# Kernel tuning notes

Hardware: AMD Instinct MI355X
Metric: run time of the kernel (lower is better)

Reference implementation:

```python
import math
import jax, jax.numpy as jnp
import numpy as np

L, H, C, T_MAX, V = 4, 12, 768, 1024, 50257
D = C // H
EPS = 1e-5


def setup_inputs() -> dict:
    key = jax.random.key(0)
    ks = iter(jax.random.split(key, 32))
    s = 0.02
    inp = {
        "idx": jax.random.randint(next(ks), (2, 1024), 0, V, dtype=jnp.int32),
        "wte": jax.random.normal(next(ks), (V, C), jnp.float32) * s,
        "wpe": jax.random.normal(next(ks), (T_MAX, C), jnp.float32) * s,
        # per-layer stacked params, weights stored [in, out]
        "ln1_w": jnp.ones((L, C), jnp.float32),
        "ln1_b": jnp.zeros((L, C), jnp.float32),
        "qkv_w": jax.random.normal(next(ks), (L, C, 3 * C), jnp.float32) * s,
        "qkv_b": jnp.zeros((L, 3 * C), jnp.float32),
        "proj_w": jax.random.normal(next(ks), (L, C, C), jnp.float32) * (s / math.sqrt(2 * L)),
        "proj_b": jnp.zeros((L, C), jnp.float32),
        "ln2_w": jnp.ones((L, C), jnp.float32),
        "ln2_b": jnp.zeros((L, C), jnp.float32),
        "fc_w": jax.random.normal(next(ks), (L, C, 4 * C), jnp.float32) * s,
        "fc_b": jnp.zeros((L, 4 * C), jnp.float32),
        "fc2_w": jax.random.normal(next(ks), (L, 4 * C, C), jnp.float32) * (s / math.sqrt(2 * L)),
        "fc2_b": jnp.zeros((L, C), jnp.float32),
        "lnf_w": jnp.ones((C,), jnp.float32),
        "lnf_b": jnp.zeros((C,), jnp.float32),
        "head_w": jax.random.normal(next(ks), (C, V), jnp.float32) * s,
    }
    return inp


def _layernorm(x, w, b):
    mu = jnp.mean(x, axis=-1, keepdims=True)
    var = jnp.mean(jnp.square(x - mu), axis=-1, keepdims=True)
    return (x - mu) * jax.lax.rsqrt(var + EPS) * w + b


def _new_gelu(x):
    k = math.sqrt(2.0 / math.pi)
    return 0.5 * x * (1.0 + jnp.tanh(k * (x + 0.044715 * x * x * x)))


def _gpt_forward(idx, wte, wpe, layer_params, lnf_w, lnf_b, head_w):
    B, T = idx.shape
    x = wte[idx] + wpe[:T][None, :, :]  # [B, T, C]
    causal = jnp.tril(jnp.ones((T, T), bool))

    def block(x, p):
        ln1w, ln1b, qkvw, qkvb, pw, pb, ln2w, ln2b, fcw, fcb, fc2w, fc2b = p
        h = _layernorm(x, ln1w, ln1b)
        qkv = h @ qkvw + qkvb  # [B, T, 3C]
        q, k, v = jnp.split(qkv, 3, axis=-1)
        # [B, H, T, D]
        q = q.reshape(B, T, H, D).transpose(0, 2, 1, 3)
        k = k.reshape(B, T, H, D).transpose(0, 2, 1, 3)
        v = v.reshape(B, T, H, D).transpose(0, 2, 1, 3)
        att = jnp.einsum("bhtd,bhsd->bhts", q, k) * (1.0 / math.sqrt(D))
        att = jnp.where(causal, att, -jnp.inf)
        att = jax.nn.softmax(att, axis=-1)
        y = jnp.einsum("bhts,bhsd->bhtd", att, v)
        y = y.transpose(0, 2, 1, 3).reshape(B, T, C)
        x = x + (y @ pw + pb)
        h2 = _layernorm(x, ln2w, ln2b)
        m = _new_gelu(h2 @ fcw + fcb) @ fc2w + fc2b
        return x + m, None

    x, _ = jax.lax.scan(block, x, layer_params)
    x = _layernorm(x, lnf_w, lnf_b)
    logits = x @ head_w  # [B, T, V]
    return logits.reshape(B * T, V)


def reference(idx, wte, wpe, ln1_w, ln1_b, qkv_w, qkv_b, proj_w, proj_b,
              ln2_w, ln2_b, fc_w, fc_b, fc2_w, fc2_b, lnf_w, lnf_b, head_w):
    layer_params = (ln1_w, ln1_b, qkv_w, qkv_b, proj_w, proj_b,
                    ln2_w, ln2_b, fc_w, fc_b, fc2_w, fc2_b)
    return _gpt_forward(idx, wte, wpe, layer_params, lnf_w, lnf_b, head_w)
```

## Files before the change

kernel.cpp:

```cpp
#include <hip/hip_runtime.h>
#include <hip/hip_bf16.h>

typedef __hip_bfloat16 bf16;
typedef __attribute__((ext_vector_type(8))) short bf16x8;
typedef __attribute__((ext_vector_type(4))) float f32x4;
typedef __attribute__((ext_vector_type(4), aligned(4))) float f32x4u;

#define NL 4
#define NH 12
#define C 768
#define T 1024
#define NB 2
#define BTOK 2048
#define V 50257
#define DH 64

__device__ __forceinline__ void gload16(const void* g, void* l) {
  __builtin_amdgcn_global_load_lds(
      (const __attribute__((address_space(1))) void*)g,
      (__attribute__((address_space(3))) void*)l, 16, 0, 0);
}

__device__ __forceinline__ float block_sum(float v, float* red) {
#pragma unroll
  for (int off = 32; off; off >>= 1) v += __shfl_down(v, off);
  int lane = threadIdx.x & 63, wid = threadIdx.x >> 6;
  __syncthreads();
  if (lane == 0) red[wid] = v;
  __syncthreads();
  return red[0] + red[1] + red[2] + red[3];
}

__global__ __launch_bounds__(256) void k_embed(const int* __restrict__ idx,
    const float* __restrict__ wte, const float* __restrict__ wpe,
    float* __restrict__ x) {
  long i = (long)blockIdx.x * 256 + threadIdx.x;
  int bt = (int)(i / C), c = (int)(i % C);
  int t = bt & (T - 1);
  x[i] = wte[(long)idx[bt] * C + c] + wpe[(long)t * C + c];
}

__global__ __launch_bounds__(256) void k_transpose_bf16(const float* __restrict__ W,
    bf16* __restrict__ Wt, int K, int N) {
  __shared__ float tile[32][33];
  long zoff = (long)blockIdx.z * K * N;
  W += zoff;
  Wt += zoff;
  int n0 = blockIdx.x * 32, k0 = blockIdx.y * 32;
  int tx = threadIdx.x, ty = threadIdx.y;
#pragma unroll
  for (int i = 0; i < 4; i++) {
    int k = k0 + ty + i * 8, n = n0 + tx;
    if (k < K && n < N) tile[ty + i * 8][tx] = W[(long)k * N + n];
  }
  __syncthreads();
#pragma unroll
  for (int i = 0; i < 4; i++) {
    int n = n0 + ty + i * 8, k = k0 + tx;
    if (n < N && k < K) Wt[(long)n * K + k] = __float2bfloat16(tile[tx][ty + i * 8]);
  }
}

__global__ __launch_bounds__(256) void k_layernorm(const float* __restrict__ x,
    const float* __restrict__ w, const float* __restrict__ b, bf16* __restrict__ out) {
  __shared__ float red[4];
  long row = blockIdx.x;
  const float* xr = x + row * C;
  int t = threadIdx.x;
  float v0 = xr[t], v1 = xr[t + 256], v2 = xr[t + 512];
  float s = block_sum(v0 + v1 + v2, red);
  float mu = s * (1.0f / C);
  float d0 = v0 - mu, d1 = v1 - mu, d2 = v2 - mu;
  float vs = block_sum(d0 * d0 + d1 * d1 + d2 * d2, red);
  float inv = rsqrtf(vs * (1.0f / C) + 1e-5f);
  bf16* orow = out + row * C;
  orow[t]       = __float2bfloat16(d0 * inv * w[t]       + b[t]);
  orow[t + 256] = __float2bfloat16(d1 * inv * w[t + 256] + b[t + 256]);
  orow[t + 512] = __float2bfloat16(d2 * inv * w[t + 512] + b[t + 512]);
}

__global__ __launch_bounds__(256) void k_attn(const bf16* __restrict__ q,
    const bf16* __restrict__ k, const bf16* __restrict__ vt,
    bf16* __restrict__ yb) {
  __shared__ __align__(16) bf16 Pl[4][16][72];
  int pr = blockIdx.x, bh = blockIdx.y;
  int b = bh / NH, h = bh % NH;
  int tid = threadIdx.x, w = tid >> 6, lane = tid & 63;
  int l15 = lane & 15, hi = lane >> 4;
  const bf16* qbase = q + (long)bh * T * DH;
  const bf16* kbase = k + (long)bh * T * DH;
  const bf16* vbase = vt + (long)bh * DH * T;

  for (int s2 = 0; s2 < 2; s2++) {
    int qt = s2 ? (T / 64 - 1 - pr) : pr;
    int qrow = qt * 64 + w * 16 + l15;
    bf16x8 qf0 = *(const bf16x8*)(qbase + (long)qrow * DH + hi * 8);
    bf16x8 qf1 = *(const bf16x8*)(qbase + (long)qrow * DH + 32 + hi * 8);

    f32x4 accy[4] = {};
    float m_run = -1e30f, l_run = 0.f;

    int nkt = qt + 1;
    for (int kt = 0; kt < nkt; kt++) {
      int kv0 = kt * 64;
      f32x4 accs[4] = {};
#pragma unroll
      for (int kvi = 0; kvi < 4; kvi++) {
        const bf16* kr = kbase + (long)(kv0 + kvi * 16 + l15) * DH + hi * 8;
        bf16x8 kf0 = *(const bf16x8*)kr;
        bf16x8 kf1 = *(const bf16x8*)(kr + 32);
        accs[kvi] = __builtin_amdgcn_mfma_f32_16x16x32_bf16(kf0, qf0, accs[kvi], 0, 0, 0);
        accs[kvi] = __builtin_amdgcn_mfma_f32_16x16x32_bf16(kf1, qf1, accs[kvi], 0, 0, 0);
      }
      bool diag = (kt == qt);
      float p[4][4];
      float tmax = -1e30f;
#pragma unroll
      for (int kvi = 0; kvi < 4; kvi++)
#pragma unroll
        for (int rr = 0; rr < 4; rr++) {
          float s = accs[kvi][rr];
          if (diag && (kvi * 16 + hi * 4 + rr > w * 16 + l15)) s = -1e30f;
          p[kvi][rr] = s;
          tmax = fmaxf(tmax, s);
        }
      tmax = fmaxf(tmax, __shfl_xor(tmax, 16));
      tmax = fmaxf(tmax, __shfl_xor(tmax, 32));
      float m_new = fmaxf(m_run, tmax);
      float scl = __expf(m_run - m_new);
      float psum = 0.f;
#pragma unroll
      for (int kvi = 0; kvi < 4; kvi++)
#pragma unroll
        for (int rr = 0; rr < 4; rr++) {
          float e = __expf(p[kvi][rr] - m_new);
          p[kvi][rr] = e;
          psum += e;
        }
      psum += __shfl_xor(psum, 16);
      psum += __shfl_xor(psum, 32);
      l_run = l_run * scl + psum;
      m_run = m_new;
#pragma unroll
      for (int rr = 0; rr < 4; rr++) {
        float sy = __shfl(scl, hi * 4 + rr);
#pragma unroll
        for (int j = 0; j < 4; j++) accy[j][rr] *= sy;
      }
#pragma unroll
      for (int kvi = 0; kvi < 4; kvi++) {
        union { bf16 hh[2]; unsigned u; } pk0, pk1;
        pk0.hh[0] = __float2bfloat16(p[kvi][0]);
        pk0.hh[1] = __float2bfloat16(p[kvi][1]);
        pk1.hh[0] = __float2bfloat16(p[kvi][2]);
        pk1.hh[1] = __float2bfloat16(p[kvi][3]);
        *(unsigned*)&Pl[w][l15][kvi * 16 + hi * 4]     = pk0.u;
        *(unsigned*)&Pl[w][l15][kvi * 16 + hi * 4 + 2] = pk1.u;
      }
#pragma unroll
      for (int c = 0; c < 2; c++) {
        bf16x8 pf = *(const bf16x8*)&Pl[w][l15][c * 32 + hi * 8];
#pragma unroll
        for (int j = 0; j < 4; j++) {
          const bf16* vr = vbase + (long)(j * 16 + l15) * T + kv0 + c * 32 + hi * 8;
          bf16x8 vf = *(const bf16x8*)vr;
          accy[j] = __builtin_amdgcn_mfma_f32_16x16x32_bf16(pf, vf, accy[j], 0, 0, 0);
        }
      }
    }
    float inv = 1.0f / l_run;
#pragma unroll
    for (int rr = 0; rr < 4; rr++) {
      float li = __shfl(inv, hi * 4 + rr);
      int qg = qt * 64 + w * 16 + hi * 4 + rr;
#pragma unroll
      for (int j = 0; j < 4; j++)
        yb[((long)(b * T + qg)) * C + h * DH + j * 16 + l15] =
            __float2bfloat16(accy[j][rr] * li);
    }
  }
}

__global__ __launch_bounds__(512, 1) void k_head(const bf16* __restrict__ A,
    const bf16* __restrict__ B, float* __restrict__ Cv) {
  __shared__ __align__(16) char lds[131072];
  int hw = blockIdx.y * 8 + blockIdx.x;
  int L = (hw & 7) * 197 + (hw >> 3);
  int mt = L & 7, nt = L >> 3;
  int m0 = mt * 256, n0 = nt * 256;
  int tid = threadIdx.x, lane = tid & 63, wid = tid >> 6;
  int wm = wid >> 2, wn = wid & 3;
  int l15 = lane & 15, hi = lane >> 4, l7 = lane & 7;
  int sg = (lane & 7) ^ (lane >> 3);
  int srA = wid * 8 + (lane >> 3);
  const bf16* Ab = A + (long)(m0 + srA) * 768 + sg * 8;
  const bf16* Bb = B + (long)(n0 + srA) * 768 + sg * 8;
  auto STAGE = [&](int tile, int h) {
    char* dst = lds + (tile & 1) * 65536 + h * 16384 + wid * 1024;
    const bf16* src = (h < 2 ? Ab : Bb) + (long)((h & 1) * 128) * 768 + tile * 64;
    gload16(src, dst);
    gload16(src + 64 * 768, dst + 8192);
  };
  f32x4 acc[8][4] = {};
  STAGE(0, 0); STAGE(0, 1); STAGE(0, 2); STAGE(0, 3); STAGE(1, 0);
  asm volatile("s_waitcnt vmcnt(2)" ::: "memory");
  __builtin_amdgcn_s_barrier();
  int bro = (wn & 1) * 64;
  int g0 = (hi ^ l7) * 16, g1 = ((4 + hi) ^ l7) * 16;
  for (int t = 0; t < 12; t++) {
    char* ha = lds + (t & 1) * 65536 + wm * 16384;
    char* hb = lds + (t & 1) * 65536 + 32768 + (wn >> 1) * 16384;
    bf16x8 af[4], bv[4];
#pragma unroll
    for (int mf = 0; mf < 4; mf++)
      af[mf] = *(const bf16x8*)(ha + (mf * 16 + l15) * 128 + g0);
#pragma unroll
    for (int nf = 0; nf < 4; nf++)
      bv[nf] = *(const bf16x8*)(hb + (bro + nf * 16 + l15) * 128 + g0);
    if (t + 1 < 12) { STAGE(t + 1, 1); STAGE(t + 1, 2); }
    __builtin_amdgcn_s_barrier();
    __builtin_amdgcn_s_setprio(1);
#pragma unroll
    for (int mf = 0; mf < 4; mf++)
#pragma unroll
      for (int nf = 0; nf < 4; nf++)
        acc[mf][nf] = __builtin_amdgcn_mfma_f32_16x16x32_bf16(af[mf], bv[nf], acc[mf][nf], 0, 0, 0);
    __builtin_amdgcn_s_setprio(0);
    __builtin_amdgcn_s_barrier();
#pragma unroll
    for (int mf = 0; mf < 4; mf++)
      af[mf] = *(const bf16x8*)(ha + ((mf + 4) * 16 + l15) * 128 + g0);
    if (t + 1 < 12) STAGE(t + 1, 3);
    __builtin_amdgcn_s_barrier();
    __builtin_amdgcn_s_setprio(1);
#pragma unroll
    for (int mf = 0; mf < 4; mf++)
#pragma unroll
      for (int nf = 0; nf < 4; nf++)
        acc[mf + 4][nf] = __builtin_amdgcn_mfma_f32_16x16x32_bf16(af[mf], bv[nf], acc[mf + 4][nf], 0, 0, 0);
    __builtin_amdgcn_s_setprio(0);
    __builtin_amdgcn_s_barrier();
#pragma unroll
    for (int mf = 0; mf < 4; mf++)
      af[mf] = *(const bf16x8*)(ha + (mf * 16 + l15) * 128 + g1);
#pragma unroll
    for (int nf = 0; nf < 4; nf++)
      bv[nf] = *(const bf16x8*)(hb + (bro + nf * 16 + l15) * 128 + g1);
    __builtin_amdgcn_s_barrier();
    __builtin_amdgcn_s_setprio(1);
#pragma unroll
    for (int mf = 0; mf < 4; mf++)
#pragma unroll
      for (int nf = 0; nf < 4; nf++)
        acc[mf][nf] = __builtin_amdgcn_mfma_f32_16x16x32_bf16(af[mf], bv[nf], acc[mf][nf], 0, 0, 0);
    __builtin_amdgcn_s_setprio(0);
    __builtin_amdgcn_s_barrier();
#pragma unroll
    for (int mf = 0; mf < 4; mf++)
      af[mf] = *(const bf16x8*)(ha + ((mf + 4) * 16 + l15) * 128 + g1);
    if (t + 2 < 12) STAGE(t + 2, 0);
    __builtin_amdgcn_s_barrier();
    __builtin_amdgcn_s_setprio(1);
#pragma unroll
    for (int mf = 0; mf < 4; mf++)
#pragma unroll
      for (int nf = 0; nf < 4; nf++)
        acc[mf + 4][nf] = __builtin_amdgcn_mfma_f32_16x16x32_bf16(af[mf], bv[nf], acc[mf + 4][nf], 0, 0, 0);
    __builtin_amdgcn_s_setprio(0);
    if (t < 11) {
      if (t + 2 < 12) asm volatile("s_waitcnt vmcnt(2)" ::: "memory");
      else            asm volatile("s_waitcnt vmcnt(0)" ::: "memory");
      __builtin_amdgcn_s_barrier();
    }
  }
  __syncthreads();
  float* Cst = (float*)lds;
#pragma unroll
  for (int rnd = 0; rnd < 4; rnd++) {
#pragma unroll
    for (int mfl = 0; mfl < 2; mfl++) {
      int mf = rnd * 2 + mfl;
#pragma unroll
      for (int nf = 0; nf < 4; nf++)
#pragma unroll
        for (int rr = 0; rr < 4; rr++)
          Cst[(wm * 32 + mfl * 16 + hi * 4 + rr) * 260 + wn * 64 + nf * 16 + l15] =
              acc[mf][nf][rr];
    }
    __syncthreads();
#pragma unroll
    for (int s = 0; s < 8; s++) {
      int gid = tid + s * 512;
      int r = gid >> 6, g = gid & 63;
      int grow = m0 + (r >> 5) * 128 + (rnd * 2 + ((r >> 4) & 1)) * 16 + (r & 15);
      int gcol = n0 + g * 4;
      f32x4 vv = *(const f32x4*)&Cst[r * 260 + g * 4];
      float* dst = Cv + (long)grow * V + gcol;
      if (gcol + 3 < V) {
        *(f32x4u*)dst = vv;
      } else {
#pragma unroll
        for (int e = 0; e < 4; e++)
          if (gcol + e < V) dst[e] = vv[e];
      }
    }
    __syncthreads();
  }
}

#define SBK 64
template <int EPI>
__global__ __launch_bounds__(256) void k_gemm_s(const bf16* __restrict__ A,
    const bf16* __restrict__ B, const float* __restrict__ bias,
    void* __restrict__ Cv, int M, int N, int K, int lda, int ldb, int ldc,
    void* __restrict__ Cv2, void* __restrict__ Cv3) {
  __shared__ __align__(16) bf16 As[2][64][SBK];
  __shared__ __align__(16) bf16 Bs[2][128][SBK];
  int nwg = gridDim.x * gridDim.y;
  int hw = blockIdx.y * gridDim.x + blockIdx.x;
  int logical = (hw & 7) * (nwg >> 3) + (hw >> 3);
  int bx = logical % gridDim.x, by = logical / gridDim.x;
  int m0 = bx * 64, n0 = by * 128;
  int tid = threadIdx.x;
  int lane = tid & 63, w = tid >> 6;
  int l15 = lane & 15, hi = lane >> 4, l7 = lane & 7;
  int srow = lane >> 3;
  int sgr = lane & 7;
  int scol = ((sgr ^ srow) << 3);
  f32x4 acc[4][2] = {};
  const bf16* Ag = A + (long)(m0 + w * 8 + srow) * lda + scol;
  const bf16* Bg = B + (long)(n0 + w * 8 + srow) * ldb + scol;
  int NT = K / SBK;
  auto STAGE = [&](int t) {
    int k0 = t * SBK, b = t & 1;
    gload16(Ag + k0,            &As[b][w * 8][0]);
    gload16(Ag + k0 + 32 * lda, &As[b][w * 8 + 32][0]);
    gload16(Bg + k0,            &Bs[b][w * 8][0]);
    gload16(Bg + k0 + 32 * ldb, &Bs[b][w * 8 + 32][0]);
    gload16(Bg + k0 + 64 * ldb, &Bs[b][w * 8 + 64][0]);
    gload16(Bg + k0 + 96 * ldb, &Bs[b][w * 8 + 96][0]);
  };
  STAGE(0);
  STAGE(1);
  int c0 = (hi ^ l7) << 3, c1 = ((4 + hi) ^ l7) << 3;
  for (int t = 0; t < NT; t++) {
    int b = t & 1;
    if (t + 1 < NT) asm volatile("s_waitcnt vmcnt(6)" ::: "memory");
    else            asm volatile("s_waitcnt vmcnt(0)" ::: "memory");
    __builtin_amdgcn_s_barrier();
    bf16x8 a0[4], a1[4], b0[2], b1[2];
#pragma unroll
    for (int i = 0; i < 4; i++) {
      a0[i] = *(const bf16x8*)&As[b][i * 16 + l15][c0];
      a1[i] = *(const bf16x8*)&As[b][i * 16 + l15][c1];
    }
#pragma unroll
    for (int j = 0; j < 2; j++) {
      b0[j] = *(const bf16x8*)&Bs[b][w * 32 + j * 16 + l15][c0];
      b1[j] = *(const bf16x8*)&Bs[b][w * 32 + j * 16 + l15][c1];
    }
    asm volatile("s_waitcnt lgkmcnt(0)" ::: "memory");
    __builtin_amdgcn_s_barrier();
    if (t + 2 < NT) STAGE(t + 2);
    __builtin_amdgcn_s_setprio(1);
#pragma unroll
    for (int i = 0; i < 4; i++)
#pragma unroll
      for (int j = 0; j < 2; j++) {
        acc[i][j] = __builtin_amdgcn_mfma_f32_16x16x32_bf16(a0[i], b0[j], acc[i][j], 0, 0, 0);
        acc[i][j] = __builtin_amdgcn_mfma_f32_16x16x32_bf16(a1[i], b1[j], acc[i][j], 0, 0, 0);
      }
    __builtin_amdgcn_s_setprio(0);
  }
#pragma unroll
  for (int j = 0; j < 2; j++) {
    int gn = n0 + w * 32 + j * 16 + l15;
    float bv = bias[gn];
#pragma unroll
    for (int i = 0; i < 4; i++)
#pragma unroll
      for (int rr = 0; rr < 4; rr++) {
        int gm = m0 + i * 16 + hi * 4 + rr;
        float v = acc[i][j][rr] + bv;
        if constexpr (EPI == 3) {
          long off = (long)gm * ldc + gn;
          ((float*)Cv)[off] = v + ((float*)Cv)[off];
        } else if constexpr (EPI == 2) {
          float u = 0.7978845608028654f * (v + 0.044715f * v * v * v);
          u = fminf(fmaxf(u, -15.f), 15.f);
          float e2 = __expf(2.f * u);
          float th = (e2 - 1.f) / (e2 + 1.f);
          ((bf16*)Cv)[(long)gm * ldc + gn] = __float2bfloat16(0.5f * v * (1.f + th));
        } else if constexpr (EPI == 5) {
          int gb = gm >> 10, gt = gm & 1023;
          int which = gn / C;
          int r = gn - which * C;
          int h = r >> 6, d = r & 63;
          long bh = (long)(gb * NH + h);
          if (which == 0)
            ((bf16*)Cv)[(bh * T + gt) * DH + d] = __float2bfloat16(v * 0.125f);
          else if (which == 1)
            ((bf16*)Cv2)[(bh * T + gt) * DH + d] = __float2bfloat16(v);
          else
            ((bf16*)Cv3)[(bh * DH + d) * T + gt] = __float2bfloat16(v);
        }
      }
  }
}

extern "C" void kernel_launch(void* const* d_in, const int* in_sizes, int n_in,
                              void* d_out, int out_size, void* d_ws, size_t ws_size,
                              hipStream_t stream) {
  const int*   idx    = (const int*)d_in[0];
  const float* wte    = (const float*)d_in[1];
  const float* wpe    = (const float*)d_in[2];
  const float* ln1_w  = (const float*)d_in[3];
  const float* ln1_b  = (const float*)d_in[4];
  const float* qkv_w  = (const float*)d_in[5];
  const float* qkv_b  = (const float*)d_in[6];
  const float* proj_w = (const float*)d_in[7];
  const float* proj_b = (const float*)d_in[8];
  const float* ln2_w  = (const float*)d_in[9];
  const float* ln2_b  = (const float*)d_in[10];
  const float* fc_w   = (const float*)d_in[11];
  const float* fc_b   = (const float*)d_in[12];
  const float* fc2_w  = (const float*)d_in[13];
  const float* fc2_b  = (const float*)d_in[14];
  const float* lnf_w  = (const float*)d_in[15];
  const float* lnf_b  = (const float*)d_in[16];
  const float* head_w = (const float*)d_in[17];
  (void)in_sizes; (void)n_in; (void)out_size; (void)ws_size;

  char* base = (char*)d_ws;
  size_t off = 0;
  auto alloc = [&](size_t bytes) -> void* {
    void* p = base + off;
    off = (off + bytes + 255) & ~(size_t)255;
    return p;
  };
  bf16* wt_qkv  = (bf16*)alloc((size_t)NL * 3 * C * C * 2);
  bf16* wt_proj = (bf16*)alloc((size_t)NL * C * C * 2);
  bf16* wt_fc   = (bf16*)alloc((size_t)NL * 4 * C * C * 2);
  bf16* wt_fc2  = (bf16*)alloc((size_t)NL * 4 * C * C * 2);
  bf16* wt_head = (bf16*)alloc((size_t)V * C * 2);
  float* x      = (float*)alloc((size_t)BTOK * C * 4);
  bf16*  xb     = (bf16*)alloc((size_t)BTOK * C * 2);
  bf16*  qb     = (bf16*)alloc((size_t)NB * NH * T * DH * 2);
  bf16*  kb     = (bf16*)alloc((size_t)NB * NH * T * DH * 2);
  bf16*  vtb    = (bf16*)alloc((size_t)NB * NH * T * DH * 2);
  bf16*  yb     = (bf16*)alloc((size_t)BTOK * C * 2);
  bf16*  mbuf   = (bf16*)alloc((size_t)BTOK * 4 * C * 2);

  dim3 tb(32, 8);
  k_transpose_bf16<<<dim3(72, 24, NL), tb, 0, stream>>>(qkv_w, wt_qkv, C, 3 * C);
  k_transpose_bf16<<<dim3(24, 24, NL), tb, 0, stream>>>(proj_w, wt_proj, C, C);
  k_transpose_bf16<<<dim3(96, 24, NL), tb, 0, stream>>>(fc_w, wt_fc, C, 4 * C);
  k_transpose_bf16<<<dim3(24, 96, NL), tb, 0, stream>>>(fc2_w, wt_fc2, 4 * C, C);
  k_transpose_bf16<<<dim3((V + 31) / 32, 24, 1), tb, 0, stream>>>(head_w, wt_head, C, V);

  k_embed<<<BTOK * C / 256, 256, 0, stream>>>(idx, wte, wpe, x);

  for (int l = 0; l < NL; l++) {
    k_layernorm<<<BTOK, 256, 0, stream>>>(x, ln1_w + l * C, ln1_b + l * C, xb);
    k_gemm_s<5><<<dim3(32, 18), 256, 0, stream>>>(xb, wt_qkv + (long)l * 3 * C * C,
        qkv_b + l * 3 * C, qb, BTOK, 3 * C, C, C, C, 0, kb, vtb);
    k_attn<<<dim3(T / 128, NB * NH), 256, 0, stream>>>(qb, kb, vtb, yb);
    k_gemm_s<3><<<dim3(32, 6), 256, 0, stream>>>(yb, wt_proj + (long)l * C * C,
        proj_b + l * C, x, BTOK, C, C, C, C, C, nullptr, nullptr);
    k_layernorm<<<BTOK, 256, 0, stream>>>(x, ln2_w + l * C, ln2_b + l * C, xb);
    k_gemm_s<2><<<dim3(32, 24), 256, 0, stream>>>(xb, wt_fc + (long)l * 4 * C * C,
        fc_b + l * 4 * C, mbuf, BTOK, 4 * C, C, C, C, 4 * C, nullptr, nullptr);
    k_gemm_s<3><<<dim3(32, 6), 256, 0, stream>>>(mbuf, wt_fc2 + (long)l * 4 * C * C,
        fc2_b + l * C, x, BTOK, C, 4 * C, 4 * C, 4 * C, C, nullptr, nullptr);
  }
  k_layernorm<<<BTOK, 256, 0, stream>>>(x, lnf_w, lnf_b, xb);
  k_head<<<dim3(8, 197), 512, 0, stream>>>(xb, wt_head, (float*)d_out);
}
```

Measured before the change: 1.073 ms.

## Split attention causal pairs across grid z and replace head GEMM with 128x128 tiles

The attention kernel stops looping over two query tiles per block and puts each one in its own block via a third grid dimension, which doubles the block count and raises parallelism. The large 256x256 LM-head GEMM kernel (512 threads, one block per CU, 128KB LDS) is replaced by a simpler 128x128 tile kernel using 256 threads with launch bounds allowing two blocks per CU. That kernel uses a double-buffered global-to-LDS pipeline and an LDS-staged epilogue. The smaller head tiles give more blocks and occupancy but less reuse per block, and the separate attention blocks lose the load balancing that pairing short and long causal tiles provided.

```diff
diff --git a/kernel.cpp b/kernel.cpp
--- a/kernel.cpp
+++ b/kernel.cpp
@@ -91,217 +91,176 @@
   const bf16* kbase = k + (long)bh * T * DH;
   const bf16* vbase = vt + (long)bh * DH * T;
 
-  for (int s2 = 0; s2 < 2; s2++) {
-    int qt = s2 ? (T / 64 - 1 - pr) : pr;
-    int qrow = qt * 64 + w * 16 + l15;
-    bf16x8 qf0 = *(const bf16x8*)(qbase + (long)qrow * DH + hi * 8);
-    bf16x8 qf1 = *(const bf16x8*)(qbase + (long)qrow * DH + 32 + hi * 8);
-
-    f32x4 accy[4] = {};
-    float m_run = -1e30f, l_run = 0.f;
-
-    int nkt = qt + 1;
-    for (int kt = 0; kt < nkt; kt++) {
-      int kv0 = kt * 64;
-      f32x4 accs[4] = {};
-#pragma unroll
-      for (int kvi = 0; kvi < 4; kvi++) {
-        const bf16* kr = kbase + (long)(kv0 + kvi * 16 + l15) * DH + hi * 8;
-        bf16x8 kf0 = *(const bf16x8*)kr;
-        bf16x8 kf1 = *(const bf16x8*)(kr + 32);
-        accs[kvi] = __builtin_amdgcn_mfma_f32_16x16x32_bf16(kf0, qf0, accs[kvi], 0, 0, 0);
-        accs[kvi] = __builtin_amdgcn_mfma_f32_16x16x32_bf16(kf1, qf1, accs[kvi], 0, 0, 0);
-      }
-      bool diag = (kt == qt);
-      float p[4][4];
-      float tmax = -1e30f;
-#pragma unroll
-      for (int kvi = 0; kvi < 4; kvi++)
-#pragma unroll
-        for (int rr = 0; rr < 4; rr++) {
-          float s = accs[kvi][rr];
-          if (diag && (kvi * 16 + hi * 4 + rr > w * 16 + l15)) s = -1e30f;
-          p[kvi][rr] = s;
-          tmax = fmaxf(tmax, s);
-        }
-      tmax = fmaxf(tmax, __shfl_xor(tmax, 16));
-      tmax = fmaxf(tmax, __shfl_xor(tmax, 32));
-      float m_new = fmaxf(m_run, tmax);
-      float scl = __expf(m_run - m_new);
-      float psum = 0.f;
-#pragma unroll
-      for (int kvi = 0; kvi < 4; kvi++)
-#pragma unroll
-        for (int rr = 0; rr < 4; rr++) {
-          float e = __expf(p[kvi][rr] - m_new);
-          p[kvi][rr] = e;
-          psum += e;
-        }
-      psum += __shfl_xor(psum, 16);
-      psum += __shfl_xor(psum, 32);
-      l_run = l_run * scl + psum;
-      m_run = m_new;
+  int qt = blockIdx.z ? (T / 64 - 1 - pr) : pr;
+  int qrow = qt * 64 + w * 16 + l15;
+  bf16x8 qf0 = *(const bf16x8*)(qbase + (long)qrow * DH + hi * 8);
+  bf16x8 qf1 = *(const bf16x8*)(qbase + (long)qrow * DH + 32 + hi * 8);
+
+  f32x4 accy[4] = {};
+  float m_run = -1e30f, l_run = 0.f;
+
+  int nkt = qt + 1;
+  for (int kt = 0; kt < nkt; kt++) {
+    int kv0 = kt * 64;
+    f32x4 accs[4] = {};
+#pragma unroll
+    for (int kvi = 0; kvi < 4; kvi++) {
+      const bf16* kr = kbase + (long)(kv0 + kvi * 16 + l15) * DH + hi * 8;
+      bf16x8 kf0 = *(const bf16x8*)kr;
+      bf16x8 kf1 = *(const bf16x8*)(kr + 32);
+      accs[kvi] = __builtin_amdgcn_mfma_f32_16x16x32_bf16(kf0, qf0, accs[kvi], 0, 0, 0);
+      accs[kvi] = __builtin_amdgcn_mfma_f32_16x16x32_bf16(kf1, qf1, accs[kvi], 0, 0, 0);
+    }
+    bool diag = (kt == qt);
+    float p[4][4];
+    float tmax = -1e30f;
+#pragma unroll
+    for (int kvi = 0; kvi < 4; kvi++)
 #pragma unroll
       for (int rr = 0; rr < 4; rr++) {
-        float sy = __shfl(scl, hi * 4 + rr);
-#pragma unroll
-        for (int j = 0; j < 4; j++) accy[j][rr] *= sy;
-      }
-#pragma unroll
-      for (int kvi = 0; kvi < 4; kvi++) {
-        union { bf16 hh[2]; unsigned u; } pk0, pk1;
-        pk0.hh[0] = __float2bfloat16(p[kvi][0]);
-        pk0.hh[1] = __float2bfloat16(p[kvi][1]);
-        pk1.hh[0] = __float2bfloat16(p[kvi][2]);
-        pk1.hh[1] = __float2bfloat16(p[kvi][3]);
-        *(unsigned*)&Pl[w][l15][kvi * 16 + hi * 4]     = pk0.u;
-        *(unsigned*)&Pl[w][l15][kvi * 16 + hi * 4 + 2] = pk1.u;
-      }
-#pragma unroll
-      for (int c = 0; c < 2; c++) {
-        bf16x8 pf = *(const bf16x8*)&Pl[w][l15][c * 32 + hi * 8];
-#pragma unroll
-        for (int j = 0; j < 4; j++) {
-          const bf16* vr = vbase + (long)(j * 16 + l15) * T + kv0 + c * 32 + hi * 8;
-          bf16x8 vf = *(const bf16x8*)vr;
-          accy[j] = __builtin_amdgcn_mfma_f32_16x16x32_bf16(pf, vf, accy[j], 0, 0, 0);
-        }
-      }
-    }
-    float inv = 1.0f / l_run;
+        float s = accs[kvi][rr];
+        if (diag && (kvi * 16 + hi * 4 + rr > w * 16 + l15)) s = -1e30f;
+        p[kvi][rr] = s;
+        tmax = fmaxf(tmax, s);
+      }
+    tmax = fmaxf(tmax, __shfl_xor(tmax, 16));
+    tmax = fmaxf(tmax, __shfl_xor(tmax, 32));
+    float m_new = fmaxf(m_run, tmax);
+    float scl = __expf(m_run - m_new);
+    float psum = 0.f;
+#pragma unroll
+    for (int kvi = 0; kvi < 4; kvi++)
+#pragma unroll
+      for (int rr = 0; rr < 4; rr++) {
+        float e = __expf(p[kvi][rr] - m_new);
+        p[kvi][rr] = e;
+        psum += e;
+      }
+    psum += __shfl_xor(psum, 16);
+    psum += __shfl_xor(psum, 32);
+    l_run = l_run * scl + psum;
+    m_run = m_new;
 #pragma unroll
     for (int rr = 0; rr < 4; rr++) {
-      float li = __shfl(inv, hi * 4 + rr);
-      int qg = qt * 64 + w * 16 + hi * 4 + rr;
-#pragma unroll
-      for (int j = 0; j < 4; j++)
-        yb[((long)(b * T + qg)) * C + h * DH + j * 16 + l15] =
-            __float2bfloat16(accy[j][rr] * li);
-    }
-  }
-}
-
-__global__ __launch_bounds__(512, 1) void k_head(const bf16* __restrict__ A,
-    const bf16* __restrict__ B, float* __restrict__ Cv) {
-  __shared__ __align__(16) char lds[131072];
-  int hw = blockIdx.y * 8 + blockIdx.x;
-  int L = (hw & 7) * 197 + (hw >> 3);
-  int mt = L & 7, nt = L >> 3;
-  int m0 = mt * 256, n0 = nt * 256;
+      float sy = __shfl(scl, hi * 4 + rr);
+#pragma unroll
+      for (int j = 0; j < 4; j++) accy[j][rr] *= sy;
+    }
+#pragma unroll
+    for (int kvi = 0; kvi < 4; kvi++) {
+      union { bf16 hh[2]; unsigned u; } pk0, pk1;
+      pk0.hh[0] = __float2bfloat16(p[kvi][0]);
+      pk0.hh[1] = __float2bfloat16(p[kvi][1]);
+      pk1.hh[0] = __float2bfloat16(p[kvi][2]);
+      pk1.hh[1] = __float2bfloat16(p[kvi][3]);
+      *(unsigned*)&Pl[w][l15][kvi * 16 + hi * 4]     = pk0.u;
+      *(unsigned*)&Pl[w][l15][kvi * 16 + hi * 4 + 2] = pk1.u;
+    }
+#pragma unroll
+    for (int c = 0; c < 2; c++) {
+      bf16x8 pf = *(const bf16x8*)&Pl[w][l15][c * 32 + hi * 8];
+#pragma unroll
+      for (int j = 0; j < 4; j++) {
+        const bf16* vr = vbase + (long)(j * 16 + l15) * T + kv0 + c * 32 + hi * 8;
+        bf16x8 vf = *(const bf16x8*)vr;
+        accy[j] = __builtin_amdgcn_mfma_f32_16x16x32_bf16(pf, vf, accy[j], 0, 0, 0);
+      }
+    }
+  }
+  float inv = 1.0f / l_run;
+#pragma unroll
+  for (int rr = 0; rr < 4; rr++) {
+    float li = __shfl(inv, hi * 4 + rr);
+    int qg = qt * 64 + w * 16 + hi * 4 + rr;
+#pragma unroll
+    for (int j = 0; j < 4; j++)
+      yb[((long)(b * T + qg)) * C + h * DH + j * 16 + l15] =
+          __float2bfloat16(accy[j][rr] * li);
+  }
+}
+
+__global__ __launch_bounds__(256, 2) void k_gemm_b(const bf16* __restrict__ A,
+    const bf16* __restrict__ B, float* __restrict__ Cv, int N) {
+  __shared__ __align__(16) bf16 As[2][128][64];
+  __shared__ __align__(16) bf16 Bs[2][128][64];
+  int nwg = gridDim.x * gridDim.y;
+  int hw = blockIdx.y * gridDim.x + blockIdx.x;
+  int logical = (hw & 7) * (nwg >> 3) + (hw >> 3);
+  int bx = logical % gridDim.x, by = logical / gridDim.x;
+  int m0 = bx * 128, n0 = by * 128;
   int tid = threadIdx.x, lane = tid & 63, wid = tid >> 6;
-  int wm = wid >> 2, wn = wid & 3;
+  int wr = wid >> 1, wc = wid & 1;
   int l15 = lane & 15, hi = lane >> 4, l7 = lane & 7;
-  int sg = (lane & 7) ^ (lane >> 3);
-  int srA = wid * 8 + (lane >> 3);
-  const bf16* Ab = A + (long)(m0 + srA) * 768 + sg * 8;
-  const bf16* Bb = B + (long)(n0 + srA) * 768 + sg * 8;
-  auto STAGE = [&](int tile, int h) {
-    char* dst = lds + (tile & 1) * 65536 + h * 16384 + wid * 1024;
-    const bf16* src = (h < 2 ? Ab : Bb) + (long)((h & 1) * 128) * 768 + tile * 64;
-    gload16(src, dst);
-    gload16(src + 64 * 768, dst + 8192);
+  int srow = lane >> 3, sgr = lane & 7;
+  int scol = ((sgr ^ srow) << 3);
+  f32x4 acc[4][4] = {};
+  const bf16* Ag = A + (long)(m0 + wid * 8 + srow) * 768 + scol;
+  const bf16* Bg = B + (long)(n0 + wid * 8 + srow) * 768 + scol;
+  const int NT = 12;
+  auto STAGE = [&](int t) {
+    int k0 = t * 64, b = t & 1;
+#pragma unroll
+    for (int r = 0; r < 4; r++) {
+      gload16(Ag + k0 + (long)(r * 32) * 768, &As[b][wid * 8 + r * 32][0]);
+      gload16(Bg + k0 + (long)(r * 32) * 768, &Bs[b][wid * 8 + r * 32][0]);
+    }
   };
-  f32x4 acc[8][4] = {};
-  STAGE(0, 0); STAGE(0, 1); STAGE(0, 2); STAGE(0, 3); STAGE(1, 0);
-  asm volatile("s_waitcnt vmcnt(2)" ::: "memory");
-  __builtin_amdgcn_s_barrier();
-  int bro = (wn & 1) * 64;
-  int g0 = (hi ^ l7) * 16, g1 = ((4 + hi) ^ l7) * 16;
-  for (int t = 0; t < 12; t++) {
-    char* ha = lds + (t & 1) * 65536 + wm * 16384;
-    char* hb = lds + (t & 1) * 65536 + 32768 + (wn >> 1) * 16384;
-    bf16x8 af[4], bv[4];
-#pragma unroll
-    for (int mf = 0; mf < 4; mf++)
-      af[mf] = *(const bf16x8*)(ha + (mf * 16 + l15) * 128 + g0);
-#pragma unroll
-    for (int nf = 0; nf < 4; nf++)
-      bv[nf] = *(const bf16x8*)(hb + (bro + nf * 16 + l15) * 128 + g0);
-    if (t + 1 < 12) { STAGE(t + 1, 1); STAGE(t + 1, 2); }
+  STAGE(0);
+  STAGE(1);
+  int c0 = (hi ^ l7) << 3, c1 = ((4 + hi) ^ l7) << 3;
+  for (int t = 0; t < NT; t++) {
+    int b = t & 1;
+    if (t + 1 < NT) asm volatile("s_waitcnt vmcnt(8)" ::: "memory");
+    else            asm volatile("s_waitcnt vmcnt(0)" ::: "memory");
     __builtin_amdgcn_s_barrier();
+    bf16x8 a0[4], a1[4], b0[4], b1[4];
+#pragma unroll
+    for (int i = 0; i < 4; i++) {
+      a0[i] = *(const bf16x8*)&As[b][wr * 64 + i * 16 + l15][c0];
+      a1[i] = *(const bf16x8*)&As[b][wr * 64 + i * 16 + l15][c1];
+      b0[i] = *(const bf16x8*)&Bs[b][wc * 64 + i * 16 + l15][c0];
+      b1[i] = *(const bf16x8*)&Bs[b][wc * 64 + i * 16 + l15][c1];
+    }
+    asm volatile("s_waitcnt lgkmcnt(0)" ::: "memory");
+    __builtin_amdgcn_s_barrier();
+    if (t + 2 < NT) STAGE(t + 2);
     __builtin_amdgcn_s_setprio(1);
 #pragma unroll
-    for (int mf = 0; mf < 4; mf++)
-#pragma unroll
-      for (int nf = 0; nf < 4; nf++)
-        acc[mf][nf] = __builtin_amdgcn_mfma_f32_16x16x32_bf16(af[mf], bv[nf], acc[mf][nf], 0, 0, 0);
+    for (int i = 0; i < 4; i++)
+#pragma unroll
+      for (int j = 0; j < 4; j++) {
+        acc[i][j] = __builtin_amdgcn_mfma_f32_16x16x32_bf16(a0[i], b0[j], acc[i][j], 0, 0, 0);
+        acc[i][j] = __builtin_amdgcn_mfma_f32_16x16x32_bf16(a1[i], b1[j], acc[i][j], 0, 0, 0);
+      }
     __builtin_amdgcn_s_setprio(0);
-    __builtin_amdgcn_s_barrier();
-#pragma unroll
-    for (int mf = 0; mf < 4; mf++)
-      af[mf] = *(const bf16x8*)(ha + ((mf + 4) * 16 + l15) * 128 + g0);
-    if (t + 1 < 12) STAGE(t + 1, 3);
-    __builtin_amdgcn_s_barrier();
-    __builtin_amdgcn_s_setprio(1);
-#pragma unroll
-    for (int mf = 0; mf < 4; mf++)
-#pragma unroll
-      for (int nf = 0; nf < 4; nf++)
-        acc[mf + 4][nf] = __builtin_amdgcn_mfma_f32_16x16x32_bf16(af[mf], bv[nf], acc[mf + 4][nf], 0, 0, 0);
-    __builtin_amdgcn_s_setprio(0);
-    __builtin_amdgcn_s_barrier();
-#pragma unroll
-    for (int mf = 0; mf < 4; mf++)
-      af[mf] = *(const bf16x8*)(ha + (mf * 16 + l15) * 128 + g1);
-#pragma unroll
-    for (int nf = 0; nf < 4; nf++)
-      bv[nf] = *(const bf16x8*)(hb + (bro + nf * 16 + l15) * 128 + g1);
-    __builtin_amdgcn_s_barrier();
-    __builtin_amdgcn_s_setprio(1);
-#pragma unroll
-    for (int mf = 0; mf < 4; mf++)
-#pragma unroll
-      for (int nf = 0; nf < 4; nf++)
-        acc[mf][nf] = __builtin_amdgcn_mfma_f32_16x16x32_bf16(af[mf], bv[nf], acc[mf][nf], 0, 0, 0);
-    __builtin_amdgcn_s_setprio(0);
-    __builtin_amdgcn_s_barrier();
-#pragma unroll
-    for (int mf = 0; mf < 4; mf++)
-      af[mf] = *(const bf16x8*)(ha + ((mf + 4) * 16 + l15) * 128 + g1);
-    if (t + 2 < 12) STAGE(t + 2, 0);
-    __builtin_amdgcn_s_barrier();
-    __builtin_amdgcn_s_setprio(1);
-#pragma unroll
-    for (int mf = 0; mf < 4; mf++)
-#pragma unroll
-      for (int nf = 0; nf < 4; nf++)
-        acc[mf + 4][nf] = __builtin_amdgcn_mfma_f32_16x16x32_bf16(af[mf], bv[nf], acc[mf + 4][nf], 0, 0, 0);
-    __builtin_amdgcn_s_setprio(0);
-    if (t < 11) {
-      if (t + 2 < 12) asm volatile("s_waitcnt vmcnt(2)" ::: "memory");
-      else            asm volatile("s_waitcnt vmcnt(0)" ::: "memory");
-      __builtin_amdgcn_s_barrier();
-    }
-  }
+  }
+  float* Ct = (float*)&As[0][0][0];
   __syncthreads();
-  float* Cst = (float*)lds;
-#pragma unroll
-  for (int rnd = 0; rnd < 4; rnd++) {
-#pragma unroll
-    for (int mfl = 0; mfl < 2; mfl++) {
-      int mf = rnd * 2 + mfl;
-#pragma unroll
-      for (int nf = 0; nf < 4; nf++)
-#pragma unroll
-        for (int rr = 0; rr < 4; rr++)
-          Cst[(wm * 32 + mfl * 16 + hi * 4 + rr) * 260 + wn * 64 + nf * 16 + l15] =
-              acc[mf][nf][rr];
+#pragma unroll
+  for (int i = 0; i < 4; i++) {
+#pragma unroll
+    for (int j = 0; j < 4; j++) {
+      int lc = wc * 64 + j * 16 + l15;
+#pragma unroll
+      for (int rr = 0; rr < 4; rr++)
+        Ct[(wr * 16 + hi * 4 + rr) * 128 + lc] = acc[i][j][rr];
     }
     __syncthreads();
 #pragma unroll
-    for (int s = 0; s < 8; s++) {
-      int gid = tid + s * 512;
-      int r = gid >> 6, g = gid & 63;
-      int grow = m0 + (r >> 5) * 128 + (rnd * 2 + ((r >> 4) & 1)) * 16 + (r & 15);
-      int gcol = n0 + g * 4;
-      f32x4 vv = *(const f32x4*)&Cst[r * 260 + g * 4];
-      float* dst = Cv + (long)grow * V + gcol;
-      if (gcol + 3 < V) {
+    for (int s = 0; s < 4; s++) {
+      int idxq = tid + s * 256;
+      int lr = idxq >> 5;
+      int c4 = (idxq & 31) * 4;
+      int gm = m0 + (lr >> 4) * 64 + i * 16 + (lr & 15);
+      int gn = n0 + c4;
+      f32x4 vv = *(const f32x4*)&Ct[lr * 128 + c4];
+      float* dst = Cv + (long)gm * N + gn;
+      if (gn + 3 < N) {
         *(f32x4u*)dst = vv;
       } else {
 #pragma unroll
         for (int e = 0; e < 4; e++)
-          if (gcol + e < V) dst[e] = vv[e];
+          if (gn + e < N) dst[e] = vv[e];
       }
     }
     __syncthreads();
@@ -464,7 +423,7 @@
     k_layernorm<<<BTOK, 256, 0, stream>>>(x, ln1_w + l * C, ln1_b + l * C, xb);
     k_gemm_s<5><<<dim3(32, 18), 256, 0, stream>>>(xb, wt_qkv + (long)l * 3 * C * C,
         qkv_b + l * 3 * C, qb, BTOK, 3 * C, C, C, C, 0, kb, vtb);
-    k_attn<<<dim3(T / 128, NB * NH), 256, 0, stream>>>(qb, kb, vtb, yb);
+    k_attn<<<dim3(T / 128, NB * NH, 2), 256, 0, stream>>>(qb, kb, vtb, yb);
     k_gemm_s<3><<<dim3(32, 6), 256, 0, stream>>>(yb, wt_proj + (long)l * C * C,
         proj_b + l * C, x, BTOK, C, C, C, C, C, nullptr, nullptr);
     k_layernorm<<<BTOK, 256, 0, stream>>>(x, ln2_w + l * C, ln2_b + l * C, xb);
@@ -474,5 +433,5 @@
         fc2_b + l * C, x, BTOK, C, 4 * C, 4 * C, 4 * C, C, nullptr, nullptr);
   }
   k_layernorm<<<BTOK, 256, 0, stream>>>(x, lnf_w, lnf_b, xb);
-  k_head<<<dim3(8, 197), 512, 0, stream>>>(xb, wt_head, (float*)d_out);
-}
+  k_gemm_b<<<dim3(16, (V + 127) / 128), 256, 0, stream>>>(xb, wt_head, (float*)d_out, V);
+}
```

Result: no change. 1.060 ms (-1.2%).
